# Kernel optimization log

Measured on AMD Instinct MI355X. Metric: run time of the kernel, lower is better.

The kernel has to match this reference:

```python
import jax, jax.numpy as jnp
import numpy as np
import math

HEADS = 8


def setup_inputs() -> dict:
    key = jax.random.key(0)
    ks = jax.random.split(key, 6)
    B, N, H, R = 16, 1024, 512, 32
    s = lambda fan_in: 1.0 / math.sqrt(fan_in)
    return {
        "x": jax.random.normal(ks[0], (B, N, H), dtype=jnp.float32),
        "Wqkv": jax.random.normal(ks[1], (H, 3 * H), dtype=jnp.float32) * s(H),
        "bqkv": jnp.zeros((3 * H,), dtype=jnp.float32),
        "Wout": jax.random.normal(ks[2], (H, H), dtype=jnp.float32) * s(H),
        "bout": jnp.zeros((H,), dtype=jnp.float32),
        "u": jax.random.normal(ks[3], (N, R), dtype=jnp.float32) * s(R),
        "v": jax.random.normal(ks[4], (R, N), dtype=jnp.float32) * s(R),
    }


def reference(x, Wqkv, bqkv, Wout, bout, u, v):
    B, N, H = x.shape
    hd = H // HEADS
    # qkv projection -> [B, N, 3, heads, head_dim] -> split
    qkv = (x @ Wqkv + bqkv).reshape(B, N, 3, HEADS, hd)
    qkv = jnp.transpose(qkv, (2, 0, 3, 1, 4))  # [3, B, heads, N, hd]
    q, k, val = qkv[0], qkv[1], qkv[2]
    # feature map applied before the softmax branch too (as in source)
    q = jax.nn.elu(q) + 1.0
    k = jax.nn.elu(k) + 1.0
    # low-rank shared bias [N, N], broadcast over batch & heads
    bias = u @ v
    scores = jnp.einsum('bhnd,bhmd->bhnm', q, k) / math.sqrt(hd)
    attn = jax.nn.softmax(scores + bias[None, None, :, :], axis=-1)
    out = jnp.einsum('bhnm,bhme->bhne', attn, val)  # [B, heads, N, hd]
    out = jnp.transpose(out, (0, 2, 1, 3)).reshape(B, N, H)
    return out @ Wout + bout
```

## Files before the change

### kernel.cpp

```cpp
#include <hip/hip_runtime.h>
#include <hip/hip_bf16.h>

typedef unsigned short u16;
typedef __attribute__((ext_vector_type(8))) short short8;
typedef __attribute__((ext_vector_type(4))) float f32x4;
typedef __attribute__((ext_vector_type(16))) float f32x16;
typedef __attribute__((ext_vector_type(4))) int i32x4;
typedef __attribute__((ext_vector_type(2))) int i32x2;

#define MFMA16(a,b,c) __builtin_amdgcn_mfma_f32_16x16x32_bf16((a),(b),(c),0,0,0)
#define MFMA32(a,b,c) __builtin_amdgcn_mfma_f32_32x32x16_bf16((a),(b),(c),0,0,0)

__device__ __forceinline__ u16 f2bf(float f) {
  union { float f; unsigned int u; } x; x.f = f;
  unsigned int u = x.u;
  return (u16)((u + 0x7fffu + ((u >> 16) & 1u)) >> 16);
}

__device__ __forceinline__ unsigned cvtpk(float a, float b) {
  unsigned r;
  asm("v_cvt_pk_bf16_f32 %0, %1, %2" : "=v"(r) : "v"(a), "v"(b));
  return r;
}

__device__ __forceinline__ float exp2v(float x) {
  float r;
  asm("v_exp_f32 %0, %1" : "=v"(r) : "v"(x));
  return r;
}

__device__ __forceinline__ void gld16(const void* g, void* l) {
  __builtin_amdgcn_global_load_lds(
      (const __attribute__((address_space(1))) void*)g,
      (__attribute__((address_space(3))) void*)l, 16, 0, 0);
}

__global__ __launch_bounds__(256) void prep(
    const float* __restrict__ x, u16* __restrict__ xb,
    const float* __restrict__ u, u16* __restrict__ ub,
    const float* __restrict__ Wqkv, u16* __restrict__ Wqkvt,
    const float* __restrict__ Wout, u16* __restrict__ Woutt,
    const float* __restrict__ vlr, u16* __restrict__ vTb) {
  __shared__ float tile[32][33];
  int bid = blockIdx.x, tid = threadIdx.x;
  if (bid < 4112) {
    const float* in; u16* out; size_t i; float sc;
    if (bid < 4096) { in = x; out = xb; i = (size_t)bid * 256 + tid; sc = 1.f; }
    else { in = u; out = ub; i = (size_t)(bid - 4096) * 256 + tid; sc = 1.44269504f; }
    f32x4 a = *(const f32x4*)(in + i * 8);
    f32x4 b = *(const f32x4*)(in + i * 8 + 4);
    union { short8 s; u16 us[8]; } r;
    #pragma unroll
    for (int j = 0; j < 4; ++j) { r.us[j] = f2bf(a[j] * sc); r.us[4 + j] = f2bf(b[j] * sc); }
    *(short8*)&out[i * 8] = r.s;
    return;
  }
  int tb = bid - 4112;
  const float* in; u16* out; int rows, cols, bx, by;
  if (tb < 768)       { in = Wqkv; out = Wqkvt; rows = 512; cols = 1536; bx = tb % 48; by = tb / 48; }
  else if (tb < 1024) { int q = tb - 768; in = Wout; out = Woutt; rows = 512; cols = 512; bx = q % 16; by = q / 16; }
  else                { in = vlr; out = vTb; rows = 32; cols = 1024; bx = tb - 1024; by = 0; }
  int bc = bx * 32, br = by * 32;
  int tx = tid & 31, ty = tid >> 5;
  #pragma unroll
  for (int i = ty; i < 32; i += 8)
    tile[i][tx] = in[(size_t)(br + i) * cols + bc + tx];
  __syncthreads();
  #pragma unroll
  for (int i = ty; i < 32; i += 8)
    out[(size_t)(bc + i) * rows + br + tx] = f2bf(tile[tx][i]);
}

template<int MODE>
__global__ __launch_bounds__(256) void gemm128(
    const u16* __restrict__ A, const u16* __restrict__ Bt,
    const float* __restrict__ bias,
    u16* __restrict__ oq, u16* __restrict__ ok, u16* __restrict__ ov,
    float* __restrict__ fo) {
  const int K = 512;
  __shared__ __align__(16) u16 As[128 * 64];
  __shared__ __align__(16) u16 Bs[128 * 64];
  int tid = threadIdx.x;
  int w = tid >> 6, ln = tid & 63, lo = ln & 15, hi = ln >> 4;
  int wr = (w >> 1) * 64, wc = (w & 1) * 64;
  int lin = blockIdx.y * gridDim.x + blockIdx.x;
  int xcd = lin & 7, idx = lin >> 3;
  int perx = gridDim.x, rows_per = gridDim.y >> 3;
  int by = xcd * rows_per + idx / perx;
  int bx = idx % perx;
  int bm = by * 128, bn = bx * 128;

  f32x4 acc[4][4];
  #pragma unroll
  for (int m = 0; m < 4; ++m)
    #pragma unroll
    for (int n = 0; n < 4; ++n)
      acc[m][n] = (f32x4){0.f, 0.f, 0.f, 0.f};

  for (int k0 = 0; k0 < K; k0 += 64) {
    #pragma unroll
    for (int i = 0; i < 4; ++i) {
      int c = i * 256 + w * 64 + ln;
      int r = c >> 3, cc = c & 7;
      gld16(&A[(size_t)(bm + r) * K + k0 + ((cc ^ (r & 7)) << 3)], &As[c << 3]);
    }
    #pragma unroll
    for (int i = 0; i < 4; ++i) {
      int c = i * 256 + w * 64 + ln;
      int r = c >> 3, cc = c & 7;
      gld16(&Bt[(size_t)(bn + r) * K + k0 + ((cc ^ (r & 7)) << 3)], &Bs[c << 3]);
    }
    __syncthreads();
    #pragma unroll
    for (int ks = 0; ks < 2; ++ks) {
      short8 a[4], b[4];
      #pragma unroll
      for (int m = 0; m < 4; ++m) {
        int row = wr + m * 16 + lo;
        a[m] = *(const short8*)&As[row * 64 + (((ks * 4 + hi) ^ (lo & 7)) << 3)];
      }
      #pragma unroll
      for (int n = 0; n < 4; ++n) {
        int row = wc + n * 16 + lo;
        b[n] = *(const short8*)&Bs[row * 64 + (((ks * 4 + hi) ^ (lo & 7)) << 3)];
      }
      #pragma unroll
      for (int m = 0; m < 4; ++m)
        #pragma unroll
        for (int n = 0; n < 4; ++n)
          acc[m][n] = MFMA16(a[m], b[n], acc[m][n]);
    }
    __syncthreads();
  }
  #pragma unroll
  for (int m = 0; m < 4; ++m)
    #pragma unroll
    for (int n = 0; n < 4; ++n) {
      int col = bn + wc + n * 16 + lo;
      int row0 = bm + wr + m * 16 + hi * 4;
      if (MODE == 0) {
        int type = col >> 9, hd = (col >> 6) & 7, e = col & 63;
        float bv = bias[col];
        if (type < 2) {
          u16* dst = (type == 0) ? oq : ok;
          #pragma unroll
          for (int r = 0; r < 4; ++r) {
            float v = acc[m][n][r] + bv;
            v = (v > 0.f) ? (v + 1.f) : __expf(v);
            if (type == 0) v *= 0.18033688f;
            int row = row0 + r;
            dst[(size_t)(((row >> 10) << 3) + hd) * 65536 + (size_t)(row & 1023) * 64 + e] = f2bf(v);
          }
        } else {
          float v0 = acc[m][n][0] + bv, v1 = acc[m][n][1] + bv;
          float v2 = acc[m][n][2] + bv, v3 = acc[m][n][3] + bv;
          i32x2 d = {(int)cvtpk(v0, v1), (int)cvtpk(v2, v3)};
          int bidx = row0 >> 10;
          *(i32x2*)&ov[(size_t)((bidx << 3) + hd) * 65536 + (size_t)e * 1024 + (row0 & 1023)] = d;
        }
      } else {
        #pragma unroll
        for (int r = 0; r < 4; ++r)
          fo[(size_t)(row0 + r) * 512 + col] = acc[m][n][r] + bias[col];
      }
    }
}

__global__ __launch_bounds__(256, 2) void attn64q(
    const u16* __restrict__ qh, const u16* __restrict__ kh,
    const u16* __restrict__ vt, const u16* __restrict__ ub,
    const u16* __restrict__ vtb, u16* __restrict__ ob) {
  __shared__ __align__(16) u16 Ks[2][64 * 64];
  __shared__ __align__(16) u16 Vs[2][64 * 64];
  int tid = threadIdx.x;
  int w = tid >> 6, ln = tid & 63;
  int m32 = ln & 31, h = ln >> 5;
  int lin = blockIdx.y * gridDim.x + blockIdx.x;
  int xcd = lin & 7, idx = lin >> 3;
  int bh = xcd * 16 + (idx >> 2);
  int q0 = (idx & 3) * 256 + w * 64;
  size_t bhb = (size_t)bh << 16;

  short8 qf[2][4], uf[2][2];
  #pragma unroll
  for (int s = 0; s < 2; ++s) {
    int qc = q0 + s * 32 + m32;
    #pragma unroll
    for (int ks = 0; ks < 4; ++ks)
      qf[s][ks] = *(const short8*)&qh[bhb + (size_t)qc * 64 + ks * 16 + h * 8];
    #pragma unroll
    for (int k2 = 0; k2 < 2; ++k2)
      uf[s][k2] = *(const short8*)&ub[(size_t)qc * 32 + k2 * 16 + h * 8];
  }

  auto STAGE = [&](int buf, int kv) {
    #pragma unroll
    for (int i = 0; i < 2; ++i) {
      int c = i * 256 + w * 64 + ln;
      int r = c >> 3, cc = c & 7;
      gld16(&kh[bhb + (size_t)(kv + r) * 64 + ((cc ^ (r & 7)) << 3)], &Ks[buf][c << 3]);
      gld16(&vt[bhb + (size_t)r * 1024 + kv + ((cc ^ (r & 7)) << 3)], &Vs[buf][c << 3]);
    }
  };

  f32x16 o[2][2];
  #pragma unroll
  for (int s = 0; s < 2; ++s)
    #pragma unroll
    for (int e = 0; e < 2; ++e)
      #pragma unroll
      for (int i = 0; i < 16; ++i) o[s][e][i] = 0.f;
  float mrun[2] = {-3e38f, -3e38f}, lrun[2] = {0.f, 0.f};

  int cur = 0;
  STAGE(0, 0);
  __syncthreads();

  for (int t = 0; t < 16; ++t) {
    int kv = t * 64;
    if (t < 15) STAGE(cur ^ 1, kv + 64);

    short8 tf[2][2];
    #pragma unroll
    for (int k2 = 0; k2 < 2; ++k2) {
      tf[k2][0] = *(const short8*)&vtb[(size_t)(kv + m32) * 32 + k2 * 16 + h * 8];
      tf[k2][1] = *(const short8*)&vtb[(size_t)(kv + 32 + m32) * 32 + k2 * 16 + h * 8];
    }

    f32x16 sA[2][2];
    #pragma unroll
    for (int s = 0; s < 2; ++s)
      #pragma unroll
      for (int e = 0; e < 2; ++e)
        #pragma unroll
        for (int i = 0; i < 16; ++i) sA[s][e][i] = 0.f;

    __builtin_amdgcn_s_setprio(1);
    #pragma unroll
    for (int k2 = 0; k2 < 2; ++k2)
      #pragma unroll
      for (int s = 0; s < 2; ++s) {
        sA[s][0] = MFMA32(tf[k2][0], uf[s][k2], sA[s][0]);
        sA[s][1] = MFMA32(tf[k2][1], uf[s][k2], sA[s][1]);
      }
    #pragma unroll
    for (int ks = 0; ks < 4; ++ks) {
      short8 k0f = *(const short8*)&Ks[cur][m32 * 64 + (((ks * 2 + h) ^ (m32 & 7)) << 3)];
      short8 k1f = *(const short8*)&Ks[cur][(32 + m32) * 64 + (((ks * 2 + h) ^ (m32 & 7)) << 3)];
      #pragma unroll
      for (int s = 0; s < 2; ++s) {
        sA[s][0] = MFMA32(k0f, qf[s][ks], sA[s][0]);
        sA[s][1] = MFMA32(k1f, qf[s][ks], sA[s][1]);
      }
    }
    __builtin_amdgcn_s_setprio(0);

    unsigned pk[2][2][4][2];
    #pragma unroll
    for (int s = 0; s < 2; ++s) {
      float pm = fmaxf(sA[s][0][0], sA[s][0][1]);
      #pragma unroll
      for (int i = 2; i < 16; i += 2) pm = fmaxf(fmaxf(pm, sA[s][0][i]), sA[s][0][i + 1]);
      #pragma unroll
      for (int i = 0; i < 16; i += 2) pm = fmaxf(fmaxf(pm, sA[s][1][i]), sA[s][1][i + 1]);
      pm = fmaxf(pm, __shfl_xor(pm, 32));
      if (!__all(pm - mrun[s] <= 11.5f)) {
        float nm = fmaxf(mrun[s], pm);
        float al = exp2v(mrun[s] - nm);
        #pragma unroll
        for (int i = 0; i < 16; ++i) { o[s][0][i] *= al; o[s][1][i] *= al; }
        lrun[s] *= al;
        mrun[s] = nm;
      }
      float ls = 0.f;
      #pragma unroll
      for (int i = 0; i < 16; ++i) { float p = exp2v(sA[s][0][i] - mrun[s]); sA[s][0][i] = p; ls += p; }
      #pragma unroll
      for (int i = 0; i < 16; ++i) { float p = exp2v(sA[s][1][i] - mrun[s]); sA[s][1][i] = p; ls += p; }
      lrun[s] += ls;
      #pragma unroll
      for (int hf = 0; hf < 2; ++hf)
        #pragma unroll
        for (int r8 = 0; r8 < 4; ++r8) {
          pk[s][hf][r8][0] = cvtpk(sA[s][hf][r8 * 4 + 0], sA[s][hf][r8 * 4 + 1]);
          pk[s][hf][r8][1] = cvtpk(sA[s][hf][r8 * 4 + 2], sA[s][hf][r8 * 4 + 3]);
        }
    }

    #pragma unroll
    for (int ms = 0; ms < 4; ++ms) {
      int kvt = ms >> 1, msl = ms & 1;
      short8 v0 = *(const short8*)&Vs[cur][m32 * 64 + (((ms * 2 + h) ^ (m32 & 7)) << 3)];
      short8 v1 = *(const short8*)&Vs[cur][(32 + m32) * 64 + (((ms * 2 + h) ^ (m32 & 7)) << 3)];
      #pragma unroll
      for (int s = 0; s < 2; ++s) {
        unsigned a0 = pk[s][kvt][2 * msl][0], b0 = pk[s][kvt][2 * msl + 1][0];
        unsigned a1 = pk[s][kvt][2 * msl][1], b1 = pk[s][kvt][2 * msl + 1][1];
        asm("v_permlane32_swap_b32 %0, %1" : "+v"(a0), "+v"(b0));
        asm("v_permlane32_swap_b32 %0, %1" : "+v"(a1), "+v"(b1));
        union { i32x4 i; short8 s8; } pu;
        pu.i = (i32x4){(int)a0, (int)a1, (int)b0, (int)b1};
        __builtin_amdgcn_s_setprio(1);
        o[s][0] = MFMA32(v0, pu.s8, o[s][0]);
        o[s][1] = MFMA32(v1, pu.s8, o[s][1]);
        __builtin_amdgcn_s_setprio(0);
      }
    }
    __syncthreads();
    cur ^= 1;
  }

  int b = bh >> 3, hd = bh & 7;
  #pragma unroll
  for (int s = 0; s < 2; ++s) {
    float lt = lrun[s] + __shfl_xor(lrun[s], 32);
    float li = 1.f / lt;
    size_t orow = ((size_t)(b * 1024 + q0 + s * 32 + m32)) * 512 + hd * 64;
    #pragma unroll
    for (int et = 0; et < 2; ++et)
      #pragma unroll
      for (int r8 = 0; r8 < 4; ++r8) {
        float v0 = o[s][et][r8 * 4 + 0] * li;
        float v1 = o[s][et][r8 * 4 + 1] * li;
        float v2 = o[s][et][r8 * 4 + 2] * li;
        float v3 = o[s][et][r8 * 4 + 3] * li;
        i32x2 d = {(int)cvtpk(v0, v1), (int)cvtpk(v2, v3)};
        *(i32x2*)&ob[orow + et * 32 + 8 * r8 + 4 * h] = d;
      }
  }
}

extern "C" void kernel_launch(void* const* d_in, const int* in_sizes, int n_in,
                              void* d_out, int out_size, void* d_ws, size_t ws_size,
                              hipStream_t stream) {
  const float* x    = (const float*)d_in[0];
  const float* Wqkv = (const float*)d_in[1];
  const float* bqkv = (const float*)d_in[2];
  const float* Wout = (const float*)d_in[3];
  const float* bout = (const float*)d_in[4];
  const float* u    = (const float*)d_in[5];
  const float* vlr  = (const float*)d_in[6];
  float* out = (float*)d_out;

  char* ws = (char*)d_ws;
  u16* qh    = (u16*)(ws);
  u16* kh    = (u16*)(ws + 16777216);
  u16* xb    = (u16*)(ws + 33554432);
  u16* ob    = (u16*)(ws + 33554432);
  u16* vTg   = (u16*)(ws + 50331648);
  u16* Wqkvt = (u16*)(ws + 67108864);
  u16* Woutt = (u16*)(ws + 68681728);
  u16* ub    = (u16*)(ws + 69206016);
  u16* vTb   = (u16*)(ws + 69271552);

  prep<<<5168, 256, 0, stream>>>(x, xb, u, ub, Wqkv, Wqkvt, Wout, Woutt, vlr, vTb);
  gemm128<0><<<dim3(12, 128), 256, 0, stream>>>(xb, Wqkvt, bqkv, qh, kh, vTg, nullptr);
  attn64q<<<dim3(4, 128), 256, 0, stream>>>(qh, kh, vTg, ub, vTb, ob);
  gemm128<1><<<dim3(4, 128), 256, 0, stream>>>(ob, Woutt, bout, nullptr, nullptr, nullptr, out);
}
```

Measured before the change: 207.4 us.

## Software-pipeline attention: overlap next tile QK with current softmax/PV, 4-slot staging

Restructures the attention kernel so the QK^T plus low-rank bias MFMAs for tile t+1 are issued alongside the softmax and PV MFMAs of tile t, using two ping-ponged score accumulators. K/V staging goes from a double buffer to a 4-slot ring prefetched three tiles ahead. The intent is to hide MFMA latency behind exp/convert work and hide global-load latency better. In exchange it doubles LDS use to 64KB per block and raises register pressure with a second score set, which may hurt occupancy at 2 blocks/CU. The setprio hints are dropped.

Result: slower. 275.3 us (+32.7%).

```diff
diff --git a/kernel.cpp b/kernel.cpp
--- a/kernel.cpp
+++ b/kernel.cpp
@@ -166,12 +166,12 @@
     }
 }
 
-__global__ __launch_bounds__(256, 2) void attn64q(
+__global__ __launch_bounds__(256, 2) void attnpipe(
     const u16* __restrict__ qh, const u16* __restrict__ kh,
     const u16* __restrict__ vt, const u16* __restrict__ ub,
     const u16* __restrict__ vtb, u16* __restrict__ ob) {
-  __shared__ __align__(16) u16 Ks[2][64 * 64];
-  __shared__ __align__(16) u16 Vs[2][64 * 64];
+  __shared__ __align__(16) u16 Ks[4][64 * 64];
+  __shared__ __align__(16) u16 Vs[4][64 * 64];
   int tid = threadIdx.x;
   int w = tid >> 6, ln = tid & 63;
   int m32 = ln & 31, h = ln >> 5;
@@ -193,122 +193,133 @@
       uf[s][k2] = *(const short8*)&ub[(size_t)qc * 32 + k2 * 16 + h * 8];
   }
 
-  auto STAGE = [&](int buf, int kv) {
+  auto STAGE = [&](int slot, int kv) {
     #pragma unroll
     for (int i = 0; i < 2; ++i) {
       int c = i * 256 + w * 64 + ln;
       int r = c >> 3, cc = c & 7;
-      gld16(&kh[bhb + (size_t)(kv + r) * 64 + ((cc ^ (r & 7)) << 3)], &Ks[buf][c << 3]);
-      gld16(&vt[bhb + (size_t)r * 1024 + kv + ((cc ^ (r & 7)) << 3)], &Vs[buf][c << 3]);
+      gld16(&kh[bhb + (size_t)(kv + r) * 64 + ((cc ^ (r & 7)) << 3)], &Ks[slot][c << 3]);
+      gld16(&vt[bhb + (size_t)r * 1024 + kv + ((cc ^ (r & 7)) << 3)], &Vs[slot][c << 3]);
     }
   };
 
+  f32x16 zro;
+  #pragma unroll
+  for (int i = 0; i < 16; ++i) zro[i] = 0.f;
   f32x16 o[2][2];
   #pragma unroll
-  for (int s = 0; s < 2; ++s)
-    #pragma unroll
-    for (int e = 0; e < 2; ++e)
-      #pragma unroll
-      for (int i = 0; i < 16; ++i) o[s][e][i] = 0.f;
+  for (int s = 0; s < 2; ++s) { o[s][0] = zro; o[s][1] = zro; }
+  f32x16 sA[2][2], sB[2][2];
   float mrun[2] = {-3e38f, -3e38f}, lrun[2] = {0.f, 0.f};
 
-  int cur = 0;
-  STAGE(0, 0);
+#define QK_CL(TT, SN)                                                          \
+  {                                                                            \
+    const int kvn_ = ((TT) + 1) * 64;                                          \
+    const int kb_ = ((TT) + 1) & 3;                                            \
+    short8 tfa_[2], tfb_[2];                                                   \
+    _Pragma("unroll")                                                          \
+    for (int k2 = 0; k2 < 2; ++k2) {                                           \
+      tfa_[k2] = *(const short8*)&vtb[(size_t)(kvn_ + m32) * 32 + k2 * 16 + h * 8]; \
+      tfb_[k2] = *(const short8*)&vtb[(size_t)(kvn_ + 32 + m32) * 32 + k2 * 16 + h * 8]; \
+    }                                                                          \
+    _Pragma("unroll")                                                          \
+    for (int ks = 0; ks < 4; ++ks) {                                           \
+      short8 k0f_ = *(const short8*)&Ks[kb_][m32 * 64 + (((ks * 2 + h) ^ (m32 & 7)) << 3)]; \
+      short8 k1f_ = *(const short8*)&Ks[kb_][(32 + m32) * 64 + (((ks * 2 + h) ^ (m32 & 7)) << 3)]; \
+      _Pragma("unroll")                                                        \
+      for (int s = 0; s < 2; ++s) {                                            \
+        SN[s][0] = MFMA32(k0f_, qf[s][ks], (ks == 0) ? zro : SN[s][0]);        \
+        SN[s][1] = MFMA32(k1f_, qf[s][ks], (ks == 0) ? zro : SN[s][1]);        \
+      }                                                                        \
+    }                                                                          \
+    _Pragma("unroll")                                                          \
+    for (int k2 = 0; k2 < 2; ++k2)                                             \
+      _Pragma("unroll")                                                        \
+      for (int s = 0; s < 2; ++s) {                                            \
+        SN[s][0] = MFMA32(tfa_[k2], uf[s][k2], SN[s][0]);                      \
+        SN[s][1] = MFMA32(tfb_[k2], uf[s][k2], SN[s][1]);                      \
+      }                                                                        \
+  }
+
+#define SM_PV(PP, SC)                                                          \
+  {                                                                            \
+    _Pragma("unroll")                                                          \
+    for (int s = 0; s < 2; ++s) {                                              \
+      float pm = fmaxf(SC[s][0][0], SC[s][0][1]);                              \
+      _Pragma("unroll")                                                        \
+      for (int i = 2; i < 16; i += 2) pm = fmaxf(pm, fmaxf(SC[s][0][i], SC[s][0][i + 1])); \
+      _Pragma("unroll")                                                        \
+      for (int i = 0; i < 16; i += 2) pm = fmaxf(pm, fmaxf(SC[s][1][i], SC[s][1][i + 1])); \
+      pm = fmaxf(pm, __shfl_xor(pm, 32));                                      \
+      if (!__all(pm - mrun[s] <= 11.5f)) {                                     \
+        float nm = fmaxf(mrun[s], pm);                                         \
+        float al = exp2v(mrun[s] - nm);                                        \
+        _Pragma("unroll")                                                      \
+        for (int i = 0; i < 16; ++i) { o[s][0][i] *= al; o[s][1][i] *= al; }   \
+        lrun[s] *= al; mrun[s] = nm;                                           \
+      }                                                                        \
+    }                                                                          \
+    _Pragma("unroll")                                                          \
+    for (int hf = 0; hf < 2; ++hf) {                                           \
+      unsigned pk_[2][4][2];                                                   \
+      _Pragma("unroll")                                                        \
+      for (int s = 0; s < 2; ++s) {                                            \
+        float ls = 0.f;                                                        \
+        _Pragma("unroll")                                                      \
+        for (int i = 0; i < 16; ++i) { float p = exp2v(SC[s][hf][i] - mrun[s]); SC[s][hf][i] = p; ls += p; } \
+        lrun[s] += ls;                                                         \
+        _Pragma("unroll")                                                      \
+        for (int r8 = 0; r8 < 4; ++r8) {                                       \
+          pk_[s][r8][0] = cvtpk(SC[s][hf][r8 * 4 + 0], SC[s][hf][r8 * 4 + 1]); \
+          pk_[s][r8][1] = cvtpk(SC[s][hf][r8 * 4 + 2], SC[s][hf][r8 * 4 + 3]); \
+        }                                                                      \
+      }                                                                        \
+      _Pragma("unroll")                                                        \
+      for (int msl = 0; msl < 2; ++msl) {                                      \
+        const int ms_ = hf * 2 + msl;                                          \
+        short8 v0_ = *(const short8*)&Vs[PP][m32 * 64 + (((ms_ * 2 + h) ^ (m32 & 7)) << 3)]; \
+        short8 v1_ = *(const short8*)&Vs[PP][(32 + m32) * 64 + (((ms_ * 2 + h) ^ (m32 & 7)) << 3)]; \
+        _Pragma("unroll")                                                      \
+        for (int s = 0; s < 2; ++s) {                                          \
+          unsigned a0 = pk_[s][2 * msl][0], b0 = pk_[s][2 * msl + 1][0];       \
+          unsigned a1 = pk_[s][2 * msl][1], b1 = pk_[s][2 * msl + 1][1];       \
+          asm("v_permlane32_swap_b32 %0, %1" : "+v"(a0), "+v"(b0));            \
+          asm("v_permlane32_swap_b32 %0, %1" : "+v"(a1), "+v"(b1));            \
+          union { i32x4 i; short8 s8; } pu;                                    \
+          pu.i = (i32x4){(int)a0, (int)a1, (int)b0, (int)b1};                  \
+          o[s][0] = MFMA32(v0_, pu.s8, o[s][0]);                               \
+          o[s][1] = MFMA32(v1_, pu.s8, o[s][1]);                               \
+        }                                                                      \
+      }                                                                        \
+    }                                                                          \
+  }
+
+#define ATTN_ITER(T, SC, SN, DOSTG, DOQK)                                      \
+  {                                                                            \
+    if (DOSTG) STAGE(((T) + 3) & 3, ((T) + 3) * 64);                           \
+    if (DOQK) QK_CL((T), SN);                                                  \
+    SM_PV(((T) & 3), SC);                                                      \
+    __syncthreads();                                                           \
+  }
+
+  STAGE(0, 0); STAGE(1, 64); STAGE(2, 128);
   __syncthreads();
-
-  for (int t = 0; t < 16; ++t) {
-    int kv = t * 64;
-    if (t < 15) STAGE(cur ^ 1, kv + 64);
-
-    short8 tf[2][2];
-    #pragma unroll
-    for (int k2 = 0; k2 < 2; ++k2) {
-      tf[k2][0] = *(const short8*)&vtb[(size_t)(kv + m32) * 32 + k2 * 16 + h * 8];
-      tf[k2][1] = *(const short8*)&vtb[(size_t)(kv + 32 + m32) * 32 + k2 * 16 + h * 8];
-    }
-
-    f32x16 sA[2][2];
-    #pragma unroll
-    for (int s = 0; s < 2; ++s)
-      #pragma unroll
-      for (int e = 0; e < 2; ++e)
-        #pragma unroll
-        for (int i = 0; i < 16; ++i) sA[s][e][i] = 0.f;
-
-    __builtin_amdgcn_s_setprio(1);
-    #pragma unroll
-    for (int k2 = 0; k2 < 2; ++k2)
-      #pragma unroll
-      for (int s = 0; s < 2; ++s) {
-        sA[s][0] = MFMA32(tf[k2][0], uf[s][k2], sA[s][0]);
-        sA[s][1] = MFMA32(tf[k2][1], uf[s][k2], sA[s][1]);
-      }
-    #pragma unroll
-    for (int ks = 0; ks < 4; ++ks) {
-      short8 k0f = *(const short8*)&Ks[cur][m32 * 64 + (((ks * 2 + h) ^ (m32 & 7)) << 3)];
-      short8 k1f = *(const short8*)&Ks[cur][(32 + m32) * 64 + (((ks * 2 + h) ^ (m32 & 7)) << 3)];
-      #pragma unroll
-      for (int s = 0; s < 2; ++s) {
-        sA[s][0] = MFMA32(k0f, qf[s][ks], sA[s][0]);
-        sA[s][1] = MFMA32(k1f, qf[s][ks], sA[s][1]);
-      }
-    }
-    __builtin_amdgcn_s_setprio(0);
-
-    unsigned pk[2][2][4][2];
-    #pragma unroll
-    for (int s = 0; s < 2; ++s) {
-      float pm = fmaxf(sA[s][0][0], sA[s][0][1]);
-      #pragma unroll
-      for (int i = 2; i < 16; i += 2) pm = fmaxf(fmaxf(pm, sA[s][0][i]), sA[s][0][i + 1]);
-      #pragma unroll
-      for (int i = 0; i < 16; i += 2) pm = fmaxf(fmaxf(pm, sA[s][1][i]), sA[s][1][i + 1]);
-      pm = fmaxf(pm, __shfl_xor(pm, 32));
-      if (!__all(pm - mrun[s] <= 11.5f)) {
-        float nm = fmaxf(mrun[s], pm);
-        float al = exp2v(mrun[s] - nm);
-        #pragma unroll
-        for (int i = 0; i < 16; ++i) { o[s][0][i] *= al; o[s][1][i] *= al; }
-        lrun[s] *= al;
-        mrun[s] = nm;
-      }
-      float ls = 0.f;
-      #pragma unroll
-      for (int i = 0; i < 16; ++i) { float p = exp2v(sA[s][0][i] - mrun[s]); sA[s][0][i] = p; ls += p; }
-      #pragma unroll
-      for (int i = 0; i < 16; ++i) { float p = exp2v(sA[s][1][i] - mrun[s]); sA[s][1][i] = p; ls += p; }
-      lrun[s] += ls;
-      #pragma unroll
-      for (int hf = 0; hf < 2; ++hf)
-        #pragma unroll
-        for (int r8 = 0; r8 < 4; ++r8) {
-          pk[s][hf][r8][0] = cvtpk(sA[s][hf][r8 * 4 + 0], sA[s][hf][r8 * 4 + 1]);
-          pk[s][hf][r8][1] = cvtpk(sA[s][hf][r8 * 4 + 2], sA[s][hf][r8 * 4 + 3]);
-        }
-    }
-
-    #pragma unroll
-    for (int ms = 0; ms < 4; ++ms) {
-      int kvt = ms >> 1, msl = ms & 1;
-      short8 v0 = *(const short8*)&Vs[cur][m32 * 64 + (((ms * 2 + h) ^ (m32 & 7)) << 3)];
-      short8 v1 = *(const short8*)&Vs[cur][(32 + m32) * 64 + (((ms * 2 + h) ^ (m32 & 7)) << 3)];
-      #pragma unroll
-      for (int s = 0; s < 2; ++s) {
-        unsigned a0 = pk[s][kvt][2 * msl][0], b0 = pk[s][kvt][2 * msl + 1][0];
-        unsigned a1 = pk[s][kvt][2 * msl][1], b1 = pk[s][kvt][2 * msl + 1][1];
-        asm("v_permlane32_swap_b32 %0, %1" : "+v"(a0), "+v"(b0));
-        asm("v_permlane32_swap_b32 %0, %1" : "+v"(a1), "+v"(b1));
-        union { i32x4 i; short8 s8; } pu;
-        pu.i = (i32x4){(int)a0, (int)a1, (int)b0, (int)b1};
-        __builtin_amdgcn_s_setprio(1);
-        o[s][0] = MFMA32(v0, pu.s8, o[s][0]);
-        o[s][1] = MFMA32(v1, pu.s8, o[s][1]);
-        __builtin_amdgcn_s_setprio(0);
-      }
-    }
-    __syncthreads();
-    cur ^= 1;
-  }
+  QK_CL(-1, sA);
+
+  int t = 0;
+  #pragma unroll 1
+  for (int t2 = 0; t2 < 6; ++t2) {
+    ATTN_ITER(t, sA, sB, 1, 1); ++t;
+    ATTN_ITER(t, sB, sA, 1, 1); ++t;
+  }
+  ATTN_ITER(12, sA, sB, 1, 1);
+  ATTN_ITER(13, sB, sA, 0, 1);
+  ATTN_ITER(14, sA, sB, 0, 1);
+  ATTN_ITER(15, sB, sA, 0, 0);
+
+#undef ATTN_ITER
+#undef SM_PV
+#undef QK_CL
 
   int b = bh >> 3, hd = bh & 7;
   #pragma unroll
@@ -355,6 +366,6 @@
 
   prep<<<5168, 256, 0, stream>>>(x, xb, u, ub, Wqkv, Wqkvt, Wout, Woutt, vlr, vTb);
   gemm128<0><<<dim3(12, 128), 256, 0, stream>>>(xb, Wqkvt, bqkv, qh, kh, vTg, nullptr);
-  attn64q<<<dim3(4, 128), 256, 0, stream>>>(qh, kh, vTg, ub, vTb, ob);
+  attnpipe<<<dim3(4, 128), 256, 0, stream>>>(qh, kh, vTg, ub, vTb, ob);
   gemm128<1><<<dim3(4, 128), 256, 0, stream>>>(ob, Woutt, bout, nullptr, nullptr, nullptr, out);
 }
```
